# Optimization experiments

Hardware: AMD Instinct MI355X
Metric: run time of the kernel (lower is better)

## Reference

```python
import jax, jax.numpy as jnp
import numpy as np

HEAD_DIM = 128
Q_HEADS = 24
KV_HEADS = 8
TARGET_KV_HEADS = 32
HIDDEN = 3072


def setup_inputs() -> dict:
    key = jax.random.key(0)
    ks = jax.random.split(key, 8)
    bsz, q_len = 4, 2048
    return {
        "hidden_states": jax.random.normal(ks[0], (bsz, q_len, HIDDEN), jnp.float32),
        "rope_rotary_cos_sin": jax.random.normal(ks[1], (bsz, q_len, HEAD_DIM), jnp.float32),
        "context_lengths": jax.random.randint(ks[2], (bsz,), 0, q_len, jnp.int32),
        "kvcache_start_index": jax.random.randint(ks[3], (bsz,), 0, q_len, jnp.int32),
        "kv_cache": jax.random.normal(ks[4], (bsz, 2, KV_HEADS, 4096, HEAD_DIM), jnp.float32),
        "Wq": jax.random.normal(ks[5], (Q_HEADS * HEAD_DIM, HIDDEN), jnp.float32) * 0.02,
        "Wk": jax.random.normal(ks[6], (KV_HEADS * HEAD_DIM, HIDDEN), jnp.float32) * 0.02,
        "Wv": jax.random.normal(ks[7], (KV_HEADS * HEAD_DIM, HIDDEN), jnp.float32) * 0.02,
        "Wo": jax.random.normal(jax.random.fold_in(key, 99), (HIDDEN, Q_HEADS * HEAD_DIM), jnp.float32) * 0.02,
    }


def reference(hidden_states, rope_rotary_cos_sin, context_lengths, kvcache_start_index,
              kv_cache, Wq, Wk, Wv, Wo):
    bsz, q_len, _ = hidden_states.shape
    # QKV projections (nn.Linear, no bias): y = x @ W^T
    q = jnp.einsum('bsh,dh->bsd', hidden_states, Wq)
    k = jnp.einsum('bsh,dh->bsd', hidden_states, Wk)
    v = jnp.einsum('bsh,dh->bsd', hidden_states, Wv)
    # [b, heads, s, d]
    q = q.reshape(bsz, q_len, Q_HEADS, HEAD_DIM).transpose(0, 2, 1, 3)
    k = k.reshape(bsz, q_len, KV_HEADS, HEAD_DIM).transpose(0, 2, 1, 3)
    v = v.reshape(bsz, q_len, KV_HEADS, HEAD_DIM).transpose(0, 2, 1, 3)
    # GQA head padding: each kv head repeated `repeats` times contiguously
    repeats = TARGET_KV_HEADS // KV_HEADS
    k = jnp.repeat(k, repeats, axis=1)
    v = jnp.repeat(v, repeats, axis=1)
    qk_scale = jnp.asarray(HEAD_DIM ** -0.5, dtype=hidden_states.dtype)
    q = q * qk_scale
    # trt::fake_attention is a placeholder: returns (query.clone(), kv_cache.clone()).
    # Faithful to the source math: attn_output = scaled query; kv_cache passes through.
    attn_output = q  # [b, Q_HEADS, s, d]
    attn_output = attn_output.transpose(0, 2, 1, 3).reshape(bsz, q_len, Q_HEADS * HEAD_DIM)
    # current (3072) == o_proj.in_features (3072): no repeat/truncate branch taken
    out = jnp.einsum('bsd,od->bso', attn_output, Wo)
    return (out, kv_cache)
```

## Files before the change

### kernel.cpp

```cpp
#include <hip/hip_runtime.h>


typedef __attribute__((ext_vector_type(8))) __bf16 bf16x8;
typedef __attribute__((ext_vector_type(4))) float f32x4;

__device__ __forceinline__ unsigned short f2bf(float f) {
  union { float f; unsigned u; } v; v.f = f;
  unsigned r = v.u + 0x7fffu + ((v.u >> 16) & 1u);
  return (unsigned short)(r >> 16);
}

__global__ void cast_f32_to_bf16(const float4* __restrict__ in,
                                 ushort4* __restrict__ out, int n4) {
  int i = blockIdx.x * blockDim.x + threadIdx.x;
  int stride = gridDim.x * blockDim.x;
  for (; i < n4; i += stride) {
    float4 v = in[i];
    ushort4 o;
    o.x = f2bf(v.x); o.y = f2bf(v.y); o.z = f2bf(v.z); o.w = f2bf(v.w);
    out[i] = o;
  }
}

__global__ void transpose_cast(const float* __restrict__ in,
                               ushort* __restrict__ out, int R, int C) {
  __shared__ float tile[32][33];
  const int tc = blockIdx.x * 32;
  const int tr = blockIdx.y * 32;
  const int lx = threadIdx.x & 31;
  const int ly = threadIdx.x >> 5;
#pragma unroll
  for (int i = 0; i < 32; i += 8)
    tile[ly + i][lx] = in[(size_t)(tr + ly + i) * C + (tc + lx)];
  __syncthreads();
#pragma unroll
  for (int i = 0; i < 32; i += 8)
    out[(size_t)(tc + ly + i) * R + (tr + lx)] = f2bf(tile[lx][ly + i]);
}

typedef const __attribute__((address_space(1))) void* gptr_t;
typedef __attribute__((address_space(3))) void* lptr_t;

__device__ __forceinline__ void gload16(const void* g, void* l) {
  __builtin_amdgcn_global_load_lds((gptr_t)g, (lptr_t)l, 16, 0, 0);
}

#define BAR   do { asm volatile("" ::: "memory"); __builtin_amdgcn_s_barrier(); asm volatile("" ::: "memory"); } while (0)
#define LGKM0 asm volatile("s_waitcnt lgkmcnt(0)" ::: "memory")
#define VM(n) asm volatile("s_waitcnt vmcnt(" #n ")" ::: "memory")

template <int OUT_BF16>
__global__ __launch_bounds__(512, 2)
void gemm_p(const ushort* __restrict__ A, const ushort* __restrict__ B,
            void* __restrict__ Cv, int M, int N, int K, float scale) {
  __shared__ __align__(16) char smem[131072];

  const int t    = threadIdx.x;
  const int w    = t >> 6;
  const int lane = t & 63;
  const int wr   = w >> 2;
  const int wc   = w & 3;
  const int fr   = lane & 15;
  const int g    = lane >> 4;

  const int nwg = gridDim.x;
  const int cpx = nwg >> 3;
  const int wg  = (blockIdx.x & 7) * cpx + (blockIdx.x >> 3);
  const int nbx = N >> 8;
  const int bx  = wg % nbx, by = wg / nbx;
  const int rowBase = by * 256, colBase = bx * 256;

  const int srow = t >> 2;
  const int scol = ((t & 3) ^ ((t >> 3) & 3)) << 3;
  const ushort* Ag = A + (size_t)(rowBase + srow) * K + scol;
  const ushort* Bg = B + (size_t)(colBase + srow) * K + scol;
  const int wofs = w << 10;

#define SLOT(T) (((T) & 3) * 32768)
#define STAGE_A(kt) do { char* d_ = smem + SLOT(kt) + wofs;            \
    const ushort* s_ = Ag + (size_t)(kt) * 32;                         \
    gload16(s_, d_); gload16(s_ + (size_t)128 * K, d_ + 8192); } while (0)
#define STAGE_B(kt) do { char* d_ = smem + SLOT(kt) + 16384 + wofs;    \
    const ushort* s_ = Bg + (size_t)(kt) * 32;                         \
    gload16(s_, d_); gload16(s_ + (size_t)128 * K, d_ + 8192); } while (0)

  const int cs   = (g ^ ((fr >> 1) & 3)) << 4;
  const int aOff = (wr * 128 + fr) * 64 + cs;
  const int bOff = 16384 + (wc * 64 + fr) * 64 + cs;

#define READ_A(dst, so, MH) do {                                       \
    const char* p_ = smem + (so) + aOff + (MH) * 4096;                 \
    dst[0] = *(const bf16x8*)(p_);                                     \
    dst[1] = *(const bf16x8*)(p_ + 1024);                              \
    dst[2] = *(const bf16x8*)(p_ + 2048);                              \
    dst[3] = *(const bf16x8*)(p_ + 3072); } while (0)
#define READ_B(dst, so) do {                                           \
    const char* p_ = smem + (so) + bOff;                               \
    dst[0] = *(const bf16x8*)(p_);                                     \
    dst[1] = *(const bf16x8*)(p_ + 1024);                              \
    dst[2] = *(const bf16x8*)(p_ + 2048);                              \
    dst[3] = *(const bf16x8*)(p_ + 3072); } while (0)
#define MFMA16(MH, A4, B4) do {                                        \
    _Pragma("unroll") for (int mi_ = 0; mi_ < 4; ++mi_)                \
    _Pragma("unroll") for (int ni_ = 0; ni_ < 4; ++ni_)                \
      acc[(MH) * 4 + mi_][ni_] = __builtin_amdgcn_mfma_f32_16x16x32_bf16( \
          A4[mi_], B4[ni_], acc[(MH) * 4 + mi_][ni_], 0, 0, 0); } while (0)

  f32x4 acc[8][4];
#pragma unroll
  for (int m = 0; m < 8; ++m)
#pragma unroll
    for (int n = 0; n < 4; ++n)
      acc[m][n] = f32x4{0.f, 0.f, 0.f, 0.f};

  bf16x8 Af0[4], Af1[4], Bp[4], Bq[4];

  const int nt = K >> 5;

  STAGE_A(0); STAGE_B(0);
  STAGE_A(1); STAGE_B(1);
  VM(4);
  BAR;
  READ_A(Af0, SLOT(0), 0);
  READ_B(Bp, SLOT(0));

#define TILE_BODY(T, BC, BN_) do {                                            \
    const int so_  = SLOT(T);                                                 \
    const int so1_ = SLOT((T) + 1);                                           \
    const bool stg_ = (T) + 2 < nt;                                           \
                                                                     \
    READ_A(Af1, so_, 1);                                                      \
    if (stg_) STAGE_A((T) + 2);                                               \
    BAR; LGKM0;                                                               \
    __builtin_amdgcn_s_setprio(1); MFMA16(0, Af0, BC); __builtin_amdgcn_s_setprio(0); \
    if ((T) < nt - 2) { VM(2); } else { VM(0); }                              \
    BAR;                                                                      \
                                                                     \
    if ((T) + 1 < nt) { READ_A(Af0, so1_, 0); READ_B(BN_, so1_); }            \
    if (stg_) STAGE_B((T) + 2);                                               \
    BAR; LGKM0;                                                               \
    __builtin_amdgcn_s_setprio(1); MFMA16(1, Af1, BC); __builtin_amdgcn_s_setprio(0); \
    BAR;                                                                      \
  } while (0)

  for (int T = 0; T < nt; T += 2) {
    TILE_BODY(T, Bp, Bq);
    TILE_BODY(T + 1, Bq, Bp);
  }

#undef TILE_BODY
#undef STAGE_A
#undef STAGE_B
#undef READ_A
#undef READ_B
#undef MFMA16
#undef SLOT

  const int orow = rowBase + wr * 128 + (g << 2);
  const int ocol = colBase + wc * 64 + fr;
#pragma unroll
  for (int mi = 0; mi < 8; ++mi)
#pragma unroll
    for (int ni = 0; ni < 4; ++ni)
#pragma unroll
      for (int i = 0; i < 4; ++i) {
        const size_t idx = (size_t)(orow + mi * 16 + i) * N + (ocol + ni * 16);
        float v = acc[mi][ni][i] * scale;
        if (OUT_BF16) ((ushort*)Cv)[idx] = f2bf(v);
        else          ((float*)Cv)[idx]  = v;
      }
}

extern "C" void kernel_launch(void* const* d_in, const int* in_sizes, int n_in,
                              void* d_out, int out_size, void* d_ws, size_t ws_size,
                              hipStream_t stream) {
  const float* hs = (const float*)d_in[0];
  const float* kv = (const float*)d_in[4];
  const float* Wq = (const float*)d_in[5];
  const float* Wo = (const float*)d_in[8];

  const int M = 8192, H = 3072;
  const int OUT_ELEMS = M * H;

  float* out = (float*)d_out;

  ushort* Xb   = (ushort*)d_ws;
  ushort* Wob  = Xb + (size_t)M * H;
  ushort* WqTb = Wob + (size_t)H * H;
  ushort* Wb   = (ushort*)(out + OUT_ELEMS);

  cast_f32_to_bf16<<<2048, 256, 0, stream>>>((const float4*)hs, (ushort4*)Xb, (M * H) / 4);
  cast_f32_to_bf16<<<1024, 256, 0, stream>>>((const float4*)Wo, (ushort4*)Wob, (H * H) / 4);
  transpose_cast<<<dim3(H / 32, H / 32), 256, 0, stream>>>(Wq, WqTb, H, H);

  const float qk_scale = 0.08838834764831845f;
  gemm_p<1><<<(H / 256) * (H / 256), 512, 0, stream>>>(Wob, WqTb, (void*)Wb, H, H, H, qk_scale);
  gemm_p<0><<<(M / 256) * (H / 256), 512, 0, stream>>>(Xb, Wb, (void*)out, M, H, H, 1.0f);

  hipMemcpyAsync(out + OUT_ELEMS, kv, (size_t)in_sizes[4] * sizeof(float),
                 hipMemcpyDeviceToDevice, stream);
}
```

Measured before the change: 369.1 us.

## Retile GEMMs to fill all CUs and fuse KV-cache copy into GEMM tails

```diff
diff --git a/kernel.cpp b/kernel.cpp
--- a/kernel.cpp
+++ b/kernel.cpp
@@ -49,11 +49,16 @@
 #define LGKM0 asm volatile("s_waitcnt lgkmcnt(0)" ::: "memory")
 #define VM(n) asm volatile("s_waitcnt vmcnt(" #n ")" ::: "memory")
 
-template <int OUT_BF16>
+template <int BN, int OUT_BF16>
 __global__ __launch_bounds__(512, 2)
-void gemm_p(const ushort* __restrict__ A, const ushort* __restrict__ B,
-            void* __restrict__ Cv, int M, int N, int K, float scale) {
-  __shared__ __align__(16) char smem[131072];
+void gemm_t(const ushort* __restrict__ A, const ushort* __restrict__ B,
+            void* __restrict__ Cv, int nby, int K, int ldc, int cofs,
+            float scale,
+            const float4* __restrict__ kvsrc, float4* __restrict__ kvdst,
+            int kvblk0, int nkv4) {
+  constexpr int NB      = BN / 64;
+  constexpr int SLOT_ST = 16384 + BN * 64;
+  __shared__ __align__(16) char smem[4 * SLOT_ST];
 
   const int t    = threadIdx.x;
   const int w    = t >> 6;
@@ -66,60 +71,58 @@
   const int nwg = gridDim.x;
   const int cpx = nwg >> 3;
   const int wg  = (blockIdx.x & 7) * cpx + (blockIdx.x >> 3);
-  const int nbx = N >> 8;
-  const int bx  = wg % nbx, by = wg / nbx;
-  const int rowBase = by * 256, colBase = bx * 256;
+  const int by  = wg % nby, bx = wg / nby;
+  const int rowBase = by * 256;
+  const int bcol    = bx * BN;
+  const int ccol    = cofs + bcol;
 
   const int srow = t >> 2;
   const int scol = ((t & 3) ^ ((t >> 3) & 3)) << 3;
   const ushort* Ag = A + (size_t)(rowBase + srow) * K + scol;
-  const ushort* Bg = B + (size_t)(colBase + srow) * K + scol;
+  const ushort* Bg = B + (size_t)(bcol + srow) * K + scol;
   const int wofs = w << 10;
 
-#define SLOT(T) (((T) & 3) * 32768)
-#define STAGE_A(kt) do { char* d_ = smem + SLOT(kt) + wofs;            \
-    const ushort* s_ = Ag + (size_t)(kt) * 32;                         \
+#define SLOT(T) (((T) & 3) * SLOT_ST)
+#define STAGE_A(kt) do { char* d_ = smem + SLOT(kt) + wofs;             \
+    const ushort* s_ = Ag + (size_t)(kt) * 32;                          \
     gload16(s_, d_); gload16(s_ + (size_t)128 * K, d_ + 8192); } while (0)
-#define STAGE_B(kt) do { char* d_ = smem + SLOT(kt) + 16384 + wofs;    \
-    const ushort* s_ = Bg + (size_t)(kt) * 32;                         \
-    gload16(s_, d_); gload16(s_ + (size_t)128 * K, d_ + 8192); } while (0)
+#define STAGE_B(kt) do { char* d_ = smem + SLOT(kt) + 16384 + wofs;     \
+    const ushort* s_ = Bg + (size_t)(kt) * 32;                          \
+    gload16(s_, d_);                                                    \
+    if (BN == 256) gload16(s_ + (size_t)128 * K, d_ + 8192); } while (0)
 
   const int cs   = (g ^ ((fr >> 1) & 3)) << 4;
   const int aOff = (wr * 128 + fr) * 64 + cs;
-  const int bOff = 16384 + (wc * 64 + fr) * 64 + cs;
-
-#define READ_A(dst, so, MH) do {                                       \
-    const char* p_ = smem + (so) + aOff + (MH) * 4096;                 \
-    dst[0] = *(const bf16x8*)(p_);                                     \
-    dst[1] = *(const bf16x8*)(p_ + 1024);                              \
-    dst[2] = *(const bf16x8*)(p_ + 2048);                              \
-    dst[3] = *(const bf16x8*)(p_ + 3072); } while (0)
-#define READ_B(dst, so) do {                                           \
-    const char* p_ = smem + (so) + bOff;                               \
-    dst[0] = *(const bf16x8*)(p_);                                     \
-    dst[1] = *(const bf16x8*)(p_ + 1024);                              \
-    dst[2] = *(const bf16x8*)(p_ + 2048);                              \
-    dst[3] = *(const bf16x8*)(p_ + 3072); } while (0)
-#define MFMA16(MH, A4, B4) do {                                        \
-    _Pragma("unroll") for (int mi_ = 0; mi_ < 4; ++mi_)                \
-    _Pragma("unroll") for (int ni_ = 0; ni_ < 4; ++ni_)                \
+  const int bOff = 16384 + (wc * (BN / 4) + fr) * 64 + cs;
+
+#define READ_A(dst, so, MH) do {                                        \
+    const char* p_ = smem + (so) + aOff + (MH) * 4096;                  \
+    _Pragma("unroll") for (int i_ = 0; i_ < 4; ++i_)                    \
+      dst[i_] = *(const bf16x8*)(p_ + i_ * 1024); } while (0)
+#define READ_B(dst, so) do {                                            \
+    const char* p_ = smem + (so) + bOff;                                \
+    _Pragma("unroll") for (int i_ = 0; i_ < NB; ++i_)                   \
+      dst[i_] = *(const bf16x8*)(p_ + i_ * 1024); } while (0)
+#define MFMAQ(MH, A4, B4) do {                                          \
+    _Pragma("unroll") for (int mi_ = 0; mi_ < 4; ++mi_)                 \
+    _Pragma("unroll") for (int ni_ = 0; ni_ < NB; ++ni_)                \
       acc[(MH) * 4 + mi_][ni_] = __builtin_amdgcn_mfma_f32_16x16x32_bf16( \
           A4[mi_], B4[ni_], acc[(MH) * 4 + mi_][ni_], 0, 0, 0); } while (0)
 
-  f32x4 acc[8][4];
+  f32x4 acc[8][NB];
 #pragma unroll
   for (int m = 0; m < 8; ++m)
 #pragma unroll
-    for (int n = 0; n < 4; ++n)
+    for (int n = 0; n < NB; ++n)
       acc[m][n] = f32x4{0.f, 0.f, 0.f, 0.f};
 
-  bf16x8 Af0[4], Af1[4], Bp[4], Bq[4];
+  bf16x8 Af0[4], Af1[4], Bp[NB], Bq[NB];
 
   const int nt = K >> 5;
 
   STAGE_A(0); STAGE_B(0);
   STAGE_A(1); STAGE_B(1);
-  VM(4);
+  if (BN == 256) { VM(4); } else { VM(3); }
   BAR;
   READ_A(Af0, SLOT(0), 0);
   READ_B(Bp, SLOT(0));
@@ -132,14 +135,14 @@
     READ_A(Af1, so_, 1);                                                      \
     if (stg_) STAGE_A((T) + 2);                                               \
     BAR; LGKM0;                                                               \
-    __builtin_amdgcn_s_setprio(1); MFMA16(0, Af0, BC); __builtin_amdgcn_s_setprio(0); \
+    __builtin_amdgcn_s_setprio(1); MFMAQ(0, Af0, BC); __builtin_amdgcn_s_setprio(0); \
     if ((T) < nt - 2) { VM(2); } else { VM(0); }                              \
     BAR;                                                                      \
                                                                      \
     if ((T) + 1 < nt) { READ_A(Af0, so1_, 0); READ_B(BN_, so1_); }            \
     if (stg_) STAGE_B((T) + 2);                                               \
     BAR; LGKM0;                                                               \
-    __builtin_amdgcn_s_setprio(1); MFMA16(1, Af1, BC); __builtin_amdgcn_s_setprio(0); \
+    __builtin_amdgcn_s_setprio(1); MFMAQ(1, Af1, BC); __builtin_amdgcn_s_setprio(0); \
     BAR;                                                                      \
   } while (0)
 
@@ -153,22 +156,31 @@
 #undef STAGE_B
 #undef READ_A
 #undef READ_B
-#undef MFMA16
+#undef MFMAQ
 #undef SLOT
 
   const int orow = rowBase + wr * 128 + (g << 2);
-  const int ocol = colBase + wc * 64 + fr;
+  const int ocol = ccol + wc * (BN / 4) + fr;
 #pragma unroll
   for (int mi = 0; mi < 8; ++mi)
 #pragma unroll
-    for (int ni = 0; ni < 4; ++ni)
+    for (int ni = 0; ni < NB; ++ni)
 #pragma unroll
       for (int i = 0; i < 4; ++i) {
-        const size_t idx = (size_t)(orow + mi * 16 + i) * N + (ocol + ni * 16);
+        const size_t idx = (size_t)(orow + mi * 16 + i) * ldc + (ocol + ni * 16);
         float v = acc[mi][ni][i] * scale;
         if (OUT_BF16) ((ushort*)Cv)[idx] = f2bf(v);
         else          ((float*)Cv)[idx]  = v;
       }
+
+  if (kvdst) {
+    const int gbi = kvblk0 + blockIdx.x;
+    const int chunk = nkv4 >> 9;
+    size_t beg = (size_t)gbi * chunk + t;
+    size_t end = (gbi == 511) ? (size_t)nkv4 : (size_t)(gbi + 1) * chunk;
+    for (size_t i = beg; i < end; i += 512)
+      kvdst[i] = kvsrc[i];
+  }
 }
 
 extern "C" void kernel_launch(void* const* d_in, const int* in_sizes, int n_in,
@@ -181,22 +193,40 @@
 
   const int M = 8192, H = 3072;
   const int OUT_ELEMS = M * H;
+  const int nkv  = in_sizes[4];
+  const int nkv4 = nkv / 4;
 
   float* out = (float*)d_out;
 
   ushort* Xb   = (ushort*)d_ws;
   ushort* Wob  = Xb + (size_t)M * H;
   ushort* WqTb = Wob + (size_t)H * H;
-  ushort* Wb   = (ushort*)(out + OUT_ELEMS);
+  const size_t WS_NEED = 2ull * ((size_t)M * H + 3ull * (size_t)H * H);
+  const bool ws_ok = ws_size >= WS_NEED;
+  ushort* Wb = ws_ok ? (WqTb + (size_t)H * H) : (ushort*)(out + OUT_ELEMS);
 
   cast_f32_to_bf16<<<2048, 256, 0, stream>>>((const float4*)hs, (ushort4*)Xb, (M * H) / 4);
   cast_f32_to_bf16<<<1024, 256, 0, stream>>>((const float4*)Wo, (ushort4*)Wob, (H * H) / 4);
   transpose_cast<<<dim3(H / 32, H / 32), 256, 0, stream>>>(Wq, WqTb, H, H);
 
   const float qk_scale = 0.08838834764831845f;
-  gemm_p<1><<<(H / 256) * (H / 256), 512, 0, stream>>>(Wob, WqTb, (void*)Wb, H, H, H, qk_scale);
-  gemm_p<0><<<(M / 256) * (H / 256), 512, 0, stream>>>(Xb, Wb, (void*)out, M, H, H, 1.0f);
-
-  hipMemcpyAsync(out + OUT_ELEMS, kv, (size_t)in_sizes[4] * sizeof(float),
-                 hipMemcpyDeviceToDevice, stream);
-}
+
+  gemm_t<128, 1><<<288, 512, 0, stream>>>(
+      Wob, WqTb, (void*)Wb, H / 256, H, H, 0,
+      qk_scale, nullptr, nullptr, 0, 0);
+
+  const float4* kvs = ws_ok ? (const float4*)kv : nullptr;
+  float4* kvd = ws_ok ? (float4*)(out + OUT_ELEMS) : nullptr;
+
+  gemm_t<256, 0><<<256, 512, 0, stream>>>(
+      Xb, Wb, (void*)out, M / 256, H, H, 0,
+      1.0f, kvs, kvd, 0, nkv4);
+  gemm_t<128, 0><<<256, 512, 0, stream>>>(
+      Xb, Wb + (size_t)2048 * H, (void*)out, M / 256, H,
+      H, 2048, 1.0f, kvs, kvd, 256, nkv4);
+
+  if (!ws_ok) {
+    hipMemcpyAsync(out + OUT_ELEMS, kv, (size_t)nkv * sizeof(float),
+                   hipMemcpyDeviceToDevice, stream);
+  }
+}
```

New measurement: 418.6 us. 13.4% more time.
